# Performance work log

Hardware: AMD Instinct MI355X
Metric: run time of the kernel (lower is better)

The kernel has to match this reference:

```python
import jax, jax.numpy as jnp
import numpy as np

SIZES = (20, 20, 20, 20, 20)          # formula_oh_sizes
OH_N = sum(SIZES)                      # 100
NUM_BINS = 65536                       # spect_bin.get_num_bins()
EPS_SIZE = 1e-4                        # eps added to subset size
IN_EPS = 1e-5                          # torch InstanceNorm1d default eps


def thermometer_oh(counts):
    # StructuredOneHot with accum=True: per-element thermometer encoding.
    # counts: (N, E) element counts -> (N, sum(SIZES)) with out[j]=1 iff j < count.
    outs = [(jnp.arange(s, dtype=counts.dtype)[None, :] < counts[:, i:i + 1]).astype(jnp.float32)
            for i, s in enumerate(SIZES)]
    return jnp.concatenate(outs, axis=-1)


def inorm(x):
    # InstanceNorm1d (affine=False) as applied here: normalize over last dim per row.
    m = jnp.mean(x, axis=-1, keepdims=True)
    v = jnp.var(x, axis=-1, keepdims=True)
    return (x - m) * jax.lax.rsqrt(v + IN_EPS)


def _lin(key, fan_in, fan_out):
    k1, k2 = jax.random.split(key)
    bound = 1.0 / np.sqrt(fan_in)
    W = jax.random.uniform(k1, (fan_in, fan_out), jnp.float32, -bound, bound)
    b = jax.random.uniform(k2, (fan_out,), jnp.float32, -bound, bound)
    return W, b


def setup_inputs():
    key = jax.random.key(0)
    ks = jax.random.split(key, 12)
    B, A, GF, S, P, E, D = 8, 48, 256, 4096, 32, 5, 256
    vert_feat_in = jax.random.normal(ks[0], (B, A, GF), jnp.float32)
    vert_mask_in = jnp.ones((B, A), jnp.float32)
    elem_idx = jax.random.randint(ks[1], (B, A), 0, E)
    vert_element_oh = jax.nn.one_hot(elem_idx, E, dtype=jnp.float32)
    adj_oh = jnp.zeros((B, A, A), jnp.float32)                      # unused by forward path
    atom_subsets = jax.random.randint(ks[2], (B, S, A), 0, 2).astype(jnp.int32)
    atom_subsets_peaks = jnp.zeros((1,), jnp.float32)               # unused (mass_idx/intensity used)
    mass_idx = jax.random.randint(ks[3], (B, S, P), 0, NUM_BINS).astype(jnp.int32)
    intensity = jax.random.uniform(ks[4], (B, S, P), jnp.float32)
    combine_W, combine_b = _lin(ks[5], OH_N + GF, GF)
    l1_W, l1_b = _lin(ks[6], GF, D)
    l2a_W, l2a_b = _lin(ks[7], D, D)
    l2b_W, l2b_b = _lin(ks[8], D, D)
    score_W, score_b = _lin(ks[9], D, 1)
    return {
        'vert_feat_in': vert_feat_in, 'vert_mask_in': vert_mask_in,
        'vert_element_oh': vert_element_oh, 'adj_oh': adj_oh,
        'atom_subsets': atom_subsets, 'atom_subsets_peaks': atom_subsets_peaks,
        'mass_idx': mass_idx, 'intensity': intensity,
        'combine_W': combine_W, 'combine_b': combine_b,
        'l1_W': l1_W, 'l1_b': l1_b, 'l2a_W': l2a_W, 'l2a_b': l2a_b,
        'l2b_W': l2b_W, 'l2b_b': l2b_b, 'score_W': score_W, 'score_b': score_b,
    }


def reference(vert_feat_in, vert_mask_in, vert_element_oh, adj_oh, atom_subsets,
              atom_subsets_peaks, mass_idx, intensity,
              combine_W, combine_b, l1_W, l1_b, l2a_W, l2a_b, l2b_W, l2b_b,
              score_W, score_b):
    B, A, GF = vert_feat_in.shape
    _, S, _ = atom_subsets.shape
    subsets_f = atom_subsets.astype(jnp.float32)
    masked_vert = vert_feat_in * vert_mask_in[:, :, None]               # (B,A,GF)
    subsets_masked = subsets_f * vert_mask_in[:, None, :]               # (B,S,A)
    # weighted sum of vertex features over each subset
    sws = jnp.einsum('bag,bsa->bsg', masked_vert, subsets_masked)        # (B,S,GF)
    # per-subset element counts -> structured one-hot formula encoding
    counts = jnp.einsum('bae,bsa->bse', vert_element_oh, subsets_f)      # (B,S,E)
    pf_oh = thermometer_oh(counts.reshape(-1, counts.shape[-1])).reshape(B, S, OH_N)
    subset_size = jnp.sum(subsets_masked, axis=2) + EPS_SIZE             # (B,S)
    mean_feat = sws / subset_size[:, :, None]
    normed = inorm(mean_feat)                                            # subset_weighted_norm
    combined = jax.nn.relu(jnp.concatenate([pf_oh, normed], -1) @ combine_W + combine_b)
    x = inorm(combined)                                                  # norm_post_combine
    x = jax.nn.relu(x @ l1_W + l1_b)
    x = jax.nn.leaky_relu(x @ l2a_W + l2a_b)
    x = jax.nn.leaky_relu(x @ l2b_W + l2b_b)
    x = jax.nn.relu(x)
    x = inorm(x)                                                         # norm_pre_score
    scores = (x @ score_W + score_b)[..., 0]                             # (B,S)
    probs = jax.nn.softmax(scores, axis=-1)
    # per-batch sparse mass-matrix binning: scatter-add intensity*prob into spectral bins
    weighted = intensity * probs[:, :, None]                             # (B,S,P)
    seg = jax.vmap(lambda idx, w: jax.ops.segment_sum(w, idx, num_segments=NUM_BINS))
    spect_out = seg(mass_idx.reshape(B, -1), weighted.reshape(B, -1))    # (B,NUM_BINS)
    return spect_out, probs
```

## Files before the change

kernel.cpp:

```cpp
#include <hip/hip_runtime.h>
#include <math.h>

#define B_DIM 8
#define A_DIM 48
#define GF_DIM 256
#define S_DIM 4096
#define P_DIM 32
#define E_DIM 5
#define OHN 100
#define NBINS 65536

typedef __attribute__((ext_vector_type(8))) short short8v;
typedef __attribute__((ext_vector_type(4))) float float4v;

__device__ __forceinline__ float wave_sum(float v) {
#pragma unroll
    for (int o = 32; o; o >>= 1) v += __shfl_xor(v, o, 64);
    return v;
}
__device__ __forceinline__ float wave_max(float v) {
#pragma unroll
    for (int o = 32; o; o >>= 1) v = fmaxf(v, __shfl_xor(v, o, 64));
    return v;
}
__device__ __forceinline__ float quad16_sum(float v) {
    v += __shfl_xor(v, 1, 64); v += __shfl_xor(v, 2, 64);
    v += __shfl_xor(v, 4, 64); v += __shfl_xor(v, 8, 64);
    return v;
}
__device__ __forceinline__ unsigned short bf16_rn(float x) {
    unsigned int u = __float_as_uint(x);
    return (unsigned short)((u + 0x7FFFu + ((u >> 16) & 1u)) >> 16);
}
__device__ __forceinline__ float bf16_val(unsigned short h) {
    return __uint_as_float(((unsigned int)h) << 16);
}
__device__ __forceinline__ float4v mfma_bf16(short8v a, short8v b, float4v c) {
    return __builtin_amdgcn_mfma_f32_16x16x32_bf16(a, b, c, 0, 0, 0);
}

__global__ __launch_bounds__(256) void k_prep(
    const float* __restrict__ cW, const float* __restrict__ l1W,
    const float* __restrict__ l2aW, const float* __restrict__ l2bW,
    const float* __restrict__ vert_feat, const float* __restrict__ vert_mask,
    const float* __restrict__ elem_oh,
    short* __restrict__ wp, short* __restrict__ wv,
    float* __restrict__ maskB, int* __restrict__ eiB,
    float4* __restrict__ spect4)
{
    const int blk = blockIdx.x;
    const int tid = threadIdx.x;
    if (blk < 1152) {
        int e = blk * 256 + tid;
        int c = e >> 13;
        int i = e & 8191;
        int j    = i & 7;
        int lane = (i >> 3) & 63;
        int nt   = (i >> 9) & 1;
        int wn   = i >> 10;
        int krel = (lane >> 4) * 8 + j;
        int n    = wn * 32 + nt * 16 + (lane & 15);
        float val = 0.f;
        if (c < 12) {
            int kp = c * 32 + krel;
            if (kp < 100)       val = cW[kp * 256 + n];
            else if (kp >= 128) val = cW[(kp - 28) * 256 + n];
        } else {
            int L  = (c - 12) >> 3;
            int kc = (c - 12) & 7;
            const float* W = (L == 0) ? l1W : (L == 1) ? l2aW : l2bW;
            val = W[(kc * 32 + krel) * 256 + n];
        }
        unsigned short h = bf16_rn(val);
        float lo = val - bf16_val(h);
        int base = c * 16384 + (i & 511);
        wp[base + (wn * 4 + nt) * 512]     = (short)h;
        wp[base + (wn * 4 + 2 + nt) * 512] = (short)bf16_rn(lo);
    } else if (blk < 1664) {
        int vb = blk - 1152;
        int vc = vb >> 5;
        int i  = (vb & 31) * 256 + tid;
        int b  = vc >> 1, v = vc & 1;
        int j    = i & 7;
        int lane = (i >> 3) & 63;
        int nt   = (i >> 9) & 1;
        int wn   = i >> 10;
        int k = v * 32 + (lane >> 4) * 8 + j;
        int n = wn * 32 + nt * 16 + (lane & 15);
        float val = 0.f;
        if (k < A_DIM) {
            float mk = vert_mask[b * A_DIM + k];
            val = vert_feat[((size_t)(b * A_DIM + k)) * GF_DIM + n] * mk * mk;
        }
        unsigned short h = bf16_rn(val);
        float lo = val - bf16_val(h);
        int base = vc * 16384 + (i & 511);
        wv[base + (wn * 4 + nt) * 512]     = (short)h;
        wv[base + (wn * 4 + 2 + nt) * 512] = (short)bf16_rn(lo);
    } else if (blk == 1664) {
        for (int t = tid; t < B_DIM * A_DIM; t += 256) {
            maskB[t] = vert_mask[t];
            int ei = 0;
#pragma unroll
            for (int e = 0; e < E_DIM; ++e)
                if (elem_oh[t * E_DIM + e] > 0.5f) ei = e;
            eiB[t] = ei;
        }
    } else {
        int z = (blk - 1665) * 256 + tid;
        spect4[z] = make_float4(0.f, 0.f, 0.f, 0.f);
    }
}

#define L_XAL 16384
#define L_PS  32768
#define L_TM  33792
#define L_INV 34304
#define L_TOT 34432

template <int NKC, int ACT, bool NORM, bool SCORE, bool THERM>
__device__ __forceinline__ void layer_pass(
    short* xAh, short* xAl, float (*ps)[32], const uint4* __restrict__ tm,
    const short* __restrict__ wstream, const float* __restrict__ bias,
    const float* __restrict__ sW, const float* __restrict__ sb,
    float* __restrict__ scores, int R0)
{
    const int tid  = threadIdx.x;
    const int lane = tid & 63;
    const int wn   = tid >> 6;
    const int quad = lane >> 4;
    const int col  = lane & 15;
    const short* wbase = wstream + wn * 2048 + lane * 8;

    unsigned int tw01 = 0, tw23 = 0;
    if (THERM) {
        const int sh = quad * 8;
        uint4 t0 = tm[col];
        uint4 t1 = tm[16 + col];
        tw01 = ((t0.x >> sh) & 0xFFu)        | (((t1.x >> sh) & 0xFFu) << 8)
             | (((t0.y >> sh) & 0xFFu) << 16) | (((t1.y >> sh) & 0xFFu) << 24);
        tw23 = ((t0.z >> sh) & 0xFFu)        | (((t1.z >> sh) & 0xFFu) << 8)
             | (((t0.w >> sh) & 0xFFu) << 16) | (((t1.w >> sh) & 0xFFu) << 24);
    }

    float4v acc[2][2];
#pragma unroll
    for (int mi = 0; mi < 2; ++mi)
#pragma unroll
        for (int nt = 0; nt < 2; ++nt) acc[mi][nt] = (float4v){0.f, 0.f, 0.f, 0.f};

    short8v bh[3][2], bl[3][2];
#pragma unroll
    for (int p = 0; p < 2; ++p) {
        if (p < NKC) {
            const short* q = wbase + p * 16384;
            bh[p][0] = *(const short8v*)(q);
            bh[p][1] = *(const short8v*)(q + 512);
            bl[p][0] = *(const short8v*)(q + 1024);
            bl[p][1] = *(const short8v*)(q + 1536);
        }
    }

#pragma unroll
    for (int kc = 0; kc < NKC; ++kc) {
        const int cur = kc % 3;
        if (kc + 2 < NKC) {
            const int nxt = (kc + 2) % 3;
            const short* q = wbase + (kc + 2) * 16384;
            bh[nxt][0] = *(const short8v*)(q);
            bh[nxt][1] = *(const short8v*)(q + 512);
            bl[nxt][0] = *(const short8v*)(q + 1024);
            bl[nxt][1] = *(const short8v*)(q + 1536);
        }
        const bool isT = THERM && (kc < 4);
        short8v ah[2], al[2];
        if (isT) {
            const unsigned int w = (kc < 2) ? tw01 : tw23;
#pragma unroll
            for (int mi = 0; mi < 2; ++mi) {
                const int bb = (kc & 1) * 16 + mi * 8;
                short8v hv;
#pragma unroll
                for (int j = 0; j < 8; ++j)
                    hv[j] = (short)(((w >> (bb + j)) & 1u) ? 0x3F80 : 0);
                ah[mi] = hv;
            }
        } else {
            const int ki = THERM ? (kc - 4) : kc;
#pragma unroll
            for (int mi = 0; mi < 2; ++mi) {
                ah[mi] = *(const short8v*)(xAh + ((ki * 2 + mi) * 64 + lane) * 8);
                al[mi] = *(const short8v*)(xAl + ((ki * 2 + mi) * 64 + lane) * 8);
            }
        }
#pragma unroll
        for (int mi = 0; mi < 2; ++mi)
#pragma unroll
            for (int nt = 0; nt < 2; ++nt) {
                acc[mi][nt] = mfma_bf16(ah[mi], bh[cur][nt], acc[mi][nt]);
                acc[mi][nt] = mfma_bf16(ah[mi], bl[cur][nt], acc[mi][nt]);
                if (!isT)
                    acc[mi][nt] = mfma_bf16(al[mi], bh[cur][nt], acc[mi][nt]);
            }
    }

    float bc0 = bias[wn * 32 + col];
    float bc1 = bias[wn * 32 + 16 + col];
#pragma unroll
    for (int mi = 0; mi < 2; ++mi)
#pragma unroll
        for (int r = 0; r < 4; ++r) {
            float z0 = acc[mi][0][r] + bc0;
            float z1 = acc[mi][1][r] + bc1;
            if (ACT == 0) { z0 = fmaxf(z0, 0.f); z1 = fmaxf(z1, 0.f); }
            else { z0 = (z0 > 0.f) ? z0 : 0.01f * z0; z1 = (z1 > 0.f) ? z1 : 0.01f * z1; }
            acc[mi][0][r] = z0; acc[mi][1][r] = z1;
        }

    __syncthreads();

    if (NORM) {
        float rsum[2][4];
#pragma unroll
        for (int mi = 0; mi < 2; ++mi)
#pragma unroll
            for (int r = 0; r < 4; ++r)
                rsum[mi][r] = quad16_sum(acc[mi][0][r] + acc[mi][1][r]);
        if (col == 0) {
#pragma unroll
            for (int mi = 0; mi < 2; ++mi)
#pragma unroll
                for (int r = 0; r < 4; ++r)
                    ps[wn][mi * 16 + quad * 4 + r] = rsum[mi][r];
        }
        __syncthreads();
        float mu[2][4];
#pragma unroll
        for (int mi = 0; mi < 2; ++mi)
#pragma unroll
            for (int r = 0; r < 4; ++r) {
                int m = mi * 16 + quad * 4 + r;
                float s = 0.f;
#pragma unroll
                for (int w = 0; w < 8; ++w) s += ps[w][m];
                mu[mi][r] = s * (1.f / 256.f);
            }
        __syncthreads();
        float qs[2][4];
#pragma unroll
        for (int mi = 0; mi < 2; ++mi)
#pragma unroll
            for (int r = 0; r < 4; ++r) {
                acc[mi][0][r] -= mu[mi][r];
                acc[mi][1][r] -= mu[mi][r];
                float q = acc[mi][0][r] * acc[mi][0][r]
                        + acc[mi][1][r] * acc[mi][1][r];
                qs[mi][r] = quad16_sum(q);
            }
        if (col == 0) {
#pragma unroll
            for (int mi = 0; mi < 2; ++mi)
#pragma unroll
                for (int r = 0; r < 4; ++r)
                    ps[wn][mi * 16 + quad * 4 + r] = qs[mi][r];
        }
        __syncthreads();
#pragma unroll
        for (int mi = 0; mi < 2; ++mi)
#pragma unroll
            for (int r = 0; r < 4; ++r) {
                int m = mi * 16 + quad * 4 + r;
                float s = 0.f;
#pragma unroll
                for (int w = 0; w < 8; ++w) s += ps[w][m];
                float rsf = 1.0f / sqrtf(s * (1.f / 256.f) + 1e-5f);
                acc[mi][0][r] *= rsf;
                acc[mi][1][r] *= rsf;
            }
    }

    if (SCORE) {
        __syncthreads();
        float sv0 = sW[wn * 32 + col];
        float sv1 = sW[wn * 32 + 16 + col];
        float psu[2][4];
#pragma unroll
        for (int mi = 0; mi < 2; ++mi)
#pragma unroll
            for (int r = 0; r < 4; ++r)
                psu[mi][r] = quad16_sum(acc[mi][0][r] * sv0 + acc[mi][1][r] * sv1);
        if (col == 0) {
#pragma unroll
            for (int mi = 0; mi < 2; ++mi)
#pragma unroll
                for (int r = 0; r < 4; ++r)
                    ps[wn][mi * 16 + quad * 4 + r] = psu[mi][r];
        }
        __syncthreads();
        if (tid < 32) {
            float s = sb[0];
#pragma unroll
            for (int w = 0; w < 8; ++w) s += ps[w][tid];
            scores[R0 + tid] = s;
        }
    } else {
#pragma unroll
        for (int mi = 0; mi < 2; ++mi)
#pragma unroll
            for (int nt = 0; nt < 2; ++nt) {
                int nn0 = (nt * 16 + col) & ~1;
                int q2  = nn0 >> 3;
                int j0  = nn0 & 7;
#pragma unroll
                for (int r = 0; r < 4; ++r) {
                    float v  = acc[mi][nt][r];
                    float pv = __shfl_xor(v, 1, 64);
                    int m15 = quad * 4 + r;
                    int rowidx = (wn * 2 + mi) * 64 + q2 * 16 + m15;
                    if ((col & 1) == 0) {
                        unsigned int wd = (unsigned int)bf16_rn(v)
                                        | ((unsigned int)bf16_rn(pv) << 16);
                        ((unsigned int*)xAh)[rowidx * 4 + (j0 >> 1)] = wd;
                    } else {
                        float ls = v  - bf16_val(bf16_rn(v));
                        float lp = pv - bf16_val(bf16_rn(pv));
                        unsigned int wd = (unsigned int)bf16_rn(lp)
                                        | ((unsigned int)bf16_rn(ls) << 16);
                        ((unsigned int*)xAl)[rowidx * 4 + (j0 >> 1)] = wd;
                    }
                }
            }
        __syncthreads();
    }
}

__global__ __launch_bounds__(512, 4) void k_mlp(
    const int* __restrict__ subsets, const short* __restrict__ wprep,
    const short* __restrict__ vertB,
    const float* __restrict__ maskB, const int* __restrict__ eiB,
    const float* __restrict__ cb,  const float* __restrict__ l1b,
    const float* __restrict__ l2ab, const float* __restrict__ l2bb,
    const float* __restrict__ sW,  const float* __restrict__ sb,
    float* __restrict__ scores)
{
    __shared__ __align__(16) char smem[L_TOT];
    short*  xAh = (short*)smem;
    short*  xAl = (short*)(smem + L_XAL);
    short*  fm  = (short*)(smem + L_XAL);
    float (*ps)[32]  = (float(*)[32])(smem + L_PS);
    uint4*  tm       = (uint4*)(smem + L_TM);
    float*  invsz    = (float*)(smem + L_INV);

    const int tid  = threadIdx.x;
    const int lane = tid & 63;
    const int wn   = tid >> 6;
    const int quad = lane >> 4;
    const int col  = lane & 15;
    const int fb   = blockIdx.x;
    const int b    = fb >> 7;
    const int R0   = fb * 32;

    if (tid < 256) {
        int g  = tid;
        int lg = g & 63;
        int t2 = g >> 6;
        int kc = t2 >> 1, mi = t2 & 1;
        int m  = mi * 16 + (lg & 15);
        int k0 = kc * 32 + (lg >> 4) * 8;
        const int* srow = subsets + (size_t)(R0 + m) * A_DIM;
        short8v hv;
#pragma unroll
        for (int j = 0; j < 8; ++j) {
            int k = k0 + j;
            hv[j] = (short)((k < A_DIM && srow[k]) ? 0x3F80 : 0);
        }
        *(short8v*)(fm + g * 8) = hv;
    }

    {
        const float mymask = (lane < A_DIM) ? maskB[b * A_DIM + lane] : 0.f;
        const int   myei   = (lane < A_DIM) ? eiB[b * A_DIM + lane]   : -1;
        unsigned long long* tmw = (unsigned long long*)tm;
#pragma unroll
        for (int i = 0; i < 4; ++i) {
            int r = wn * 4 + i;
            int fl = (lane < A_DIM) ? subsets[(size_t)(R0 + r) * A_DIM + lane] : 0;
            unsigned long long m0 = __ballot(fl != 0 && myei == 0);
            unsigned long long m1 = __ballot(fl != 0 && myei == 1);
            unsigned long long m2 = __ballot(fl != 0 && myei == 2);
            unsigned long long m3 = __ballot(fl != 0 && myei == 3);
            unsigned long long m4 = __ballot(fl != 0 && myei == 4);
            float ssz = wave_sum(fl ? mymask : 0.f) + 1e-4f;
            if (lane == 0) {
                unsigned int c0 = __popcll(m0), c1 = __popcll(m1),
                             c2 = __popcll(m2), c3 = __popcll(m3),
                             c4 = __popcll(m4);
                unsigned long long r0 = (1ull << (c0 > 20u ? 20u : c0)) - 1ull;
                unsigned long long r1 = (1ull << (c1 > 20u ? 20u : c1)) - 1ull;
                unsigned long long r2 = (1ull << (c2 > 20u ? 20u : c2)) - 1ull;
                unsigned long long r3 = (1ull << (c3 > 20u ? 20u : c3)) - 1ull;
                unsigned long long r4 = (1ull << (c4 > 20u ? 20u : c4)) - 1ull;
                unsigned long long lo = r0 | (r1 << 20) | (r2 << 40) | (r3 << 60);
                unsigned long long hi = (r3 >> 4) | (r4 << 16);
                tmw[r * 2]     = lo;
                tmw[r * 2 + 1] = hi;
                invsz[r]  = 1.0f / ssz;
            }
        }
    }
    __syncthreads();

    {
        const short* wbase = vertB + b * 32768 + wn * 2048 + lane * 8;
        float4v acc[2][2];
#pragma unroll
        for (int mi = 0; mi < 2; ++mi)
#pragma unroll
            for (int nt = 0; nt < 2; ++nt) acc[mi][nt] = (float4v){0.f, 0.f, 0.f, 0.f};

        short8v bh[2][2], bl[2][2];
#pragma unroll
        for (int kc = 0; kc < 2; ++kc) {
            const short* q = wbase + kc * 16384;
            bh[kc][0] = *(const short8v*)(q);
            bh[kc][1] = *(const short8v*)(q + 512);
            bl[kc][0] = *(const short8v*)(q + 1024);
            bl[kc][1] = *(const short8v*)(q + 1536);
        }
#pragma unroll
        for (int kc = 0; kc < 2; ++kc) {
            short8v a0 = *(const short8v*)(fm + ((kc * 2 + 0) * 64 + lane) * 8);
            short8v a1 = *(const short8v*)(fm + ((kc * 2 + 1) * 64 + lane) * 8);
#pragma unroll
            for (int nt = 0; nt < 2; ++nt) {
                acc[0][nt] = mfma_bf16(a0, bh[kc][nt], acc[0][nt]);
                acc[0][nt] = mfma_bf16(a0, bl[kc][nt], acc[0][nt]);
                acc[1][nt] = mfma_bf16(a1, bh[kc][nt], acc[1][nt]);
                acc[1][nt] = mfma_bf16(a1, bl[kc][nt], acc[1][nt]);
            }
        }

#pragma unroll
        for (int mi = 0; mi < 2; ++mi)
#pragma unroll
            for (int r = 0; r < 4; ++r) {
                float iv = invsz[mi * 16 + quad * 4 + r];
                acc[mi][0][r] *= iv;
                acc[mi][1][r] *= iv;
            }

        __syncthreads();

        {
            float rsum[2][4];
#pragma unroll
            for (int mi = 0; mi < 2; ++mi)
#pragma unroll
                for (int r = 0; r < 4; ++r)
                    rsum[mi][r] = quad16_sum(acc[mi][0][r] + acc[mi][1][r]);
            if (col == 0) {
#pragma unroll
                for (int mi = 0; mi < 2; ++mi)
#pragma unroll
                    for (int r = 0; r < 4; ++r)
                        ps[wn][mi * 16 + quad * 4 + r] = rsum[mi][r];
            }
            __syncthreads();
            float mu[2][4];
#pragma unroll
            for (int mi = 0; mi < 2; ++mi)
#pragma unroll
                for (int r = 0; r < 4; ++r) {
                    int m = mi * 16 + quad * 4 + r;
                    float s = 0.f;
#pragma unroll
                    for (int w = 0; w < 8; ++w) s += ps[w][m];
                    mu[mi][r] = s * (1.f / 256.f);
                }
            __syncthreads();
            float qs[2][4];
#pragma unroll
            for (int mi = 0; mi < 2; ++mi)
#pragma unroll
                for (int r = 0; r < 4; ++r) {
                    acc[mi][0][r] -= mu[mi][r];
                    acc[mi][1][r] -= mu[mi][r];
                    float q = acc[mi][0][r] * acc[mi][0][r]
                            + acc[mi][1][r] * acc[mi][1][r];
                    qs[mi][r] = quad16_sum(q);
                }
            if (col == 0) {
#pragma unroll
                for (int mi = 0; mi < 2; ++mi)
#pragma unroll
                    for (int r = 0; r < 4; ++r)
                        ps[wn][mi * 16 + quad * 4 + r] = qs[mi][r];
            }
            __syncthreads();
#pragma unroll
            for (int mi = 0; mi < 2; ++mi)
#pragma unroll
                for (int r = 0; r < 4; ++r) {
                    int m = mi * 16 + quad * 4 + r;
                    float s = 0.f;
#pragma unroll
                    for (int w = 0; w < 8; ++w) s += ps[w][m];
                    float rsf = 1.0f / sqrtf(s * (1.f / 256.f) + 1e-5f);
                    acc[mi][0][r] *= rsf;
                    acc[mi][1][r] *= rsf;
                }
        }

#pragma unroll
        for (int mi = 0; mi < 2; ++mi)
#pragma unroll
            for (int nt = 0; nt < 2; ++nt) {
                int nn0 = (nt * 16 + col) & ~1;
                int q2  = nn0 >> 3;
                int j0  = nn0 & 7;
#pragma unroll
                for (int r = 0; r < 4; ++r) {
                    float v  = acc[mi][nt][r];
                    float pv = __shfl_xor(v, 1, 64);
                    int m15 = quad * 4 + r;
                    int rowidx = (wn * 2 + mi) * 64 + q2 * 16 + m15;
                    if ((col & 1) == 0) {
                        unsigned int wd = (unsigned int)bf16_rn(v)
                                        | ((unsigned int)bf16_rn(pv) << 16);
                        ((unsigned int*)xAh)[rowidx * 4 + (j0 >> 1)] = wd;
                    } else {
                        float ls = v  - bf16_val(bf16_rn(v));
                        float lp = pv - bf16_val(bf16_rn(pv));
                        unsigned int wd = (unsigned int)bf16_rn(lp)
                                        | ((unsigned int)bf16_rn(ls) << 16);
                        ((unsigned int*)xAl)[rowidx * 4 + (j0 >> 1)] = wd;
                    }
                }
            }
        __syncthreads();
    }

    layer_pass<12, 0, true,  false, true >(xAh, xAl, ps, tm, wprep,
        cb, nullptr, nullptr, nullptr, R0);
    layer_pass< 8, 0, false, false, false>(xAh, xAl, ps, tm, wprep + 12 * 16384,
        l1b, nullptr, nullptr, nullptr, R0);
    layer_pass< 8, 1, false, false, false>(xAh, xAl, ps, tm, wprep + 20 * 16384,
        l2ab, nullptr, nullptr, nullptr, R0);
    layer_pass< 8, 0, true,  true,  false>(xAh, xAl, ps, tm, wprep + 28 * 16384,
        l2bb, sW, sb, scores, R0);
}

__global__ __launch_bounds__(256) void k_softmax(float* __restrict__ probs) {
    const int b   = blockIdx.x;
    const int tid = threadIdx.x;
    __shared__ float redA[4];
    __shared__ float redB[4];
    float* sp = probs + (size_t)b * S_DIM;

    float v[16];
    float mx = -INFINITY;
#pragma unroll
    for (int i = 0; i < 16; ++i) {
        v[i] = sp[tid + i * 256];
        mx = fmaxf(mx, v[i]);
    }
    mx = wave_max(mx);
    if ((tid & 63) == 0) redA[tid >> 6] = mx;
    __syncthreads();
    mx = fmaxf(fmaxf(redA[0], redA[1]), fmaxf(redA[2], redA[3]));

    float sum = 0.f;
#pragma unroll
    for (int i = 0; i < 16; ++i) {
        v[i] = expf(v[i] - mx);
        sum += v[i];
    }
    sum = wave_sum(sum);
    if ((tid & 63) == 0) redB[tid >> 6] = sum;
    __syncthreads();
    float tot = redB[0] + redB[1] + redB[2] + redB[3];
    float inv = 1.0f / tot;
#pragma unroll
    for (int i = 0; i < 16; ++i) sp[tid + i * 256] = v[i] * inv;
}

__global__ __launch_bounds__(256) void k_scatter(
    const int*   __restrict__ mass_idx,
    const float* __restrict__ intensity,
    const float* __restrict__ probs,
    float* __restrict__ spect)
{
    int i  = blockIdx.x * 256 + threadIdx.x;
    int bs = i >> 5;
    int b  = i >> 17;
    float w = intensity[i] * probs[bs];
    unsafeAtomicAdd(spect + ((size_t)b << 16) + mass_idx[i], w);
}

extern "C" void kernel_launch(void* const* d_in, const int* in_sizes, int n_in,
                              void* d_out, int out_size, void* d_ws, size_t ws_size,
                              hipStream_t stream) {
    const float* vert_feat = (const float*)d_in[0];
    const float* vert_mask = (const float*)d_in[1];
    const float* elem_oh   = (const float*)d_in[2];
    const int*   subsets   = (const int*)d_in[4];
    const int*   mass_idx  = (const int*)d_in[6];
    const float* intensity = (const float*)d_in[7];
    const float* combine_W = (const float*)d_in[8];
    const float* combine_b = (const float*)d_in[9];
    const float* l1_W      = (const float*)d_in[10];
    const float* l1_b      = (const float*)d_in[11];
    const float* l2a_W     = (const float*)d_in[12];
    const float* l2a_b     = (const float*)d_in[13];
    const float* l2b_W     = (const float*)d_in[14];
    const float* l2b_b     = (const float*)d_in[15];
    const float* score_W   = (const float*)d_in[16];
    const float* score_b   = (const float*)d_in[17];

    float* out   = (float*)d_out;
    float* spect = out;
    float* probs = out + (size_t)B_DIM * NBINS;

    short* wprep = (short*)d_ws;
    short* vertB = wprep + 36 * 16384;
    float* maskB = (float*)(vertB + 16 * 16384);
    int*   eiB   = (int*)(maskB + B_DIM * A_DIM);

    k_prep<<<2177, 256, 0, stream>>>(combine_W, l1_W, l2a_W, l2b_W,
        vert_feat, vert_mask, elem_oh, wprep, vertB, maskB, eiB,
        (float4*)spect);
    k_mlp<<<1024, 512, 0, stream>>>(subsets, wprep, vertB, maskB, eiB,
        combine_b, l1_b, l2a_b, l2b_b, score_W, score_b, probs);
    k_softmax<<<B_DIM, 256, 0, stream>>>(probs);
    k_scatter<<<(B_DIM * S_DIM * P_DIM) / 256, 256, 0, stream>>>(
        mass_idx, intensity, probs, spect);
}
```

Before: 247.1 us.

## Double MLP row tile to 64 rows per block to reuse streamed weights

Each k_mlp block now processes 64 subset rows instead of 32, with each wave computing four 16-row MFMA tiles rather than two, and the grid is halved to 512 blocks. Every weight fragment loaded from global memory now feeds twice as many MFMAs, which reduces weight traffic per row. The weight prefetch depth drops from two chunks ahead to one to offset the larger accumulator and A-operand register footprint, and shared memory roughly doubles. Risks are higher register pressure and lower occupancy, fewer blocks relative to the CU count, and less latency hiding on the weight stream.

```diff
diff --git a/kernel.cpp b/kernel.cpp
--- a/kernel.cpp
+++ b/kernel.cpp
@@ -112,15 +112,15 @@
     }
 }
 
-#define L_XAL 16384
-#define L_PS  32768
-#define L_TM  33792
-#define L_INV 34304
-#define L_TOT 34432
+#define L_XAL 32768
+#define L_PS  65536
+#define L_TM  67584
+#define L_INV 68608
+#define L_TOT 68864
 
 template <int NKC, int ACT, bool NORM, bool SCORE, bool THERM>
 __device__ __forceinline__ void layer_pass(
-    short* xAh, short* xAl, float (*ps)[32], const uint4* __restrict__ tm,
+    short* xAh, short* xAl, float (*ps)[64], const uint4* __restrict__ tm,
     const short* __restrict__ wstream, const float* __restrict__ bias,
     const float* __restrict__ sW, const float* __restrict__ sb,
     float* __restrict__ scores, int R0)
@@ -132,69 +132,72 @@
     const int col  = lane & 15;
     const short* wbase = wstream + wn * 2048 + lane * 8;
 
-    unsigned int tw01 = 0, tw23 = 0;
+    unsigned int tw0 = 0, tw1 = 0, tw2 = 0, tw3 = 0;
     if (THERM) {
         const int sh = quad * 8;
         uint4 t0 = tm[col];
         uint4 t1 = tm[16 + col];
-        tw01 = ((t0.x >> sh) & 0xFFu)        | (((t1.x >> sh) & 0xFFu) << 8)
-             | (((t0.y >> sh) & 0xFFu) << 16) | (((t1.y >> sh) & 0xFFu) << 24);
-        tw23 = ((t0.z >> sh) & 0xFFu)        | (((t1.z >> sh) & 0xFFu) << 8)
-             | (((t0.w >> sh) & 0xFFu) << 16) | (((t1.w >> sh) & 0xFFu) << 24);
-    }
-
-    float4v acc[2][2];
-#pragma unroll
-    for (int mi = 0; mi < 2; ++mi)
+        uint4 t2 = tm[32 + col];
+        uint4 t3 = tm[48 + col];
+        tw0 = ((t0.x >> sh) & 0xFFu)        | (((t1.x >> sh) & 0xFFu) << 8)
+            | (((t2.x >> sh) & 0xFFu) << 16) | (((t3.x >> sh) & 0xFFu) << 24);
+        tw1 = ((t0.y >> sh) & 0xFFu)        | (((t1.y >> sh) & 0xFFu) << 8)
+            | (((t2.y >> sh) & 0xFFu) << 16) | (((t3.y >> sh) & 0xFFu) << 24);
+        tw2 = ((t0.z >> sh) & 0xFFu)        | (((t1.z >> sh) & 0xFFu) << 8)
+            | (((t2.z >> sh) & 0xFFu) << 16) | (((t3.z >> sh) & 0xFFu) << 24);
+        tw3 = ((t0.w >> sh) & 0xFFu)        | (((t1.w >> sh) & 0xFFu) << 8)
+            | (((t2.w >> sh) & 0xFFu) << 16) | (((t3.w >> sh) & 0xFFu) << 24);
+    }
+
+    float4v acc[4][2];
+#pragma unroll
+    for (int mi = 0; mi < 4; ++mi)
 #pragma unroll
         for (int nt = 0; nt < 2; ++nt) acc[mi][nt] = (float4v){0.f, 0.f, 0.f, 0.f};
 
-    short8v bh[3][2], bl[3][2];
-#pragma unroll
-    for (int p = 0; p < 2; ++p) {
-        if (p < NKC) {
-            const short* q = wbase + p * 16384;
-            bh[p][0] = *(const short8v*)(q);
-            bh[p][1] = *(const short8v*)(q + 512);
-            bl[p][0] = *(const short8v*)(q + 1024);
-            bl[p][1] = *(const short8v*)(q + 1536);
-        }
+    short8v bh[2][2], bl[2][2];
+    {
+        const short* q = wbase;
+        bh[0][0] = *(const short8v*)(q);
+        bh[0][1] = *(const short8v*)(q + 512);
+        bl[0][0] = *(const short8v*)(q + 1024);
+        bl[0][1] = *(const short8v*)(q + 1536);
     }
 
 #pragma unroll
     for (int kc = 0; kc < NKC; ++kc) {
-        const int cur = kc % 3;
-        if (kc + 2 < NKC) {
-            const int nxt = (kc + 2) % 3;
-            const short* q = wbase + (kc + 2) * 16384;
+        const int cur = kc & 1;
+        if (kc + 1 < NKC) {
+            const int nxt = (kc + 1) & 1;
+            const short* q = wbase + (kc + 1) * 16384;
             bh[nxt][0] = *(const short8v*)(q);
             bh[nxt][1] = *(const short8v*)(q + 512);
             bl[nxt][0] = *(const short8v*)(q + 1024);
             bl[nxt][1] = *(const short8v*)(q + 1536);
         }
         const bool isT = THERM && (kc < 4);
-        short8v ah[2], al[2];
+        short8v ah[4], al[4];
         if (isT) {
-            const unsigned int w = (kc < 2) ? tw01 : tw23;
-#pragma unroll
-            for (int mi = 0; mi < 2; ++mi) {
-                const int bb = (kc & 1) * 16 + mi * 8;
+            const unsigned int w = (kc == 0) ? tw0 : (kc == 1) ? tw1
+                                 : (kc == 2) ? tw2 : tw3;
+#pragma unroll
+            for (int mi = 0; mi < 4; ++mi) {
                 short8v hv;
 #pragma unroll
                 for (int j = 0; j < 8; ++j)
-                    hv[j] = (short)(((w >> (bb + j)) & 1u) ? 0x3F80 : 0);
+                    hv[j] = (short)(((w >> (mi * 8 + j)) & 1u) ? 0x3F80 : 0);
                 ah[mi] = hv;
             }
         } else {
             const int ki = THERM ? (kc - 4) : kc;
 #pragma unroll
-            for (int mi = 0; mi < 2; ++mi) {
-                ah[mi] = *(const short8v*)(xAh + ((ki * 2 + mi) * 64 + lane) * 8);
-                al[mi] = *(const short8v*)(xAl + ((ki * 2 + mi) * 64 + lane) * 8);
-            }
-        }
-#pragma unroll
-        for (int mi = 0; mi < 2; ++mi)
+            for (int mi = 0; mi < 4; ++mi) {
+                ah[mi] = *(const short8v*)(xAh + ((ki * 4 + mi) * 64 + lane) * 8);
+                al[mi] = *(const short8v*)(xAl + ((ki * 4 + mi) * 64 + lane) * 8);
+            }
+        }
+#pragma unroll
+        for (int mi = 0; mi < 4; ++mi)
 #pragma unroll
             for (int nt = 0; nt < 2; ++nt) {
                 acc[mi][nt] = mfma_bf16(ah[mi], bh[cur][nt], acc[mi][nt]);
@@ -207,7 +210,7 @@
     float bc0 = bias[wn * 32 + col];
     float bc1 = bias[wn * 32 + 16 + col];
 #pragma unroll
-    for (int mi = 0; mi < 2; ++mi)
+    for (int mi = 0; mi < 4; ++mi)
 #pragma unroll
         for (int r = 0; r < 4; ++r) {
             float z0 = acc[mi][0][r] + bc0;
@@ -220,23 +223,23 @@
     __syncthreads();
 
     if (NORM) {
-        float rsum[2][4];
-#pragma unroll
-        for (int mi = 0; mi < 2; ++mi)
+        float rsum[4][4];
+#pragma unroll
+        for (int mi = 0; mi < 4; ++mi)
 #pragma unroll
             for (int r = 0; r < 4; ++r)
                 rsum[mi][r] = quad16_sum(acc[mi][0][r] + acc[mi][1][r]);
         if (col == 0) {
 #pragma unroll
-            for (int mi = 0; mi < 2; ++mi)
+            for (int mi = 0; mi < 4; ++mi)
 #pragma unroll
                 for (int r = 0; r < 4; ++r)
                     ps[wn][mi * 16 + quad * 4 + r] = rsum[mi][r];
         }
         __syncthreads();
-        float mu[2][4];
-#pragma unroll
-        for (int mi = 0; mi < 2; ++mi)
+        float mu[4][4];
+#pragma unroll
+        for (int mi = 0; mi < 4; ++mi)
 #pragma unroll
             for (int r = 0; r < 4; ++r) {
                 int m = mi * 16 + quad * 4 + r;
@@ -246,9 +249,9 @@
                 mu[mi][r] = s * (1.f / 256.f);
             }
         __syncthreads();
-        float qs[2][4];
-#pragma unroll
-        for (int mi = 0; mi < 2; ++mi)
+        float qs[4][4];
+#pragma unroll
+        for (int mi = 0; mi < 4; ++mi)
 #pragma unroll
             for (int r = 0; r < 4; ++r) {
                 acc[mi][0][r] -= mu[mi][r];
@@ -259,14 +262,14 @@
             }
         if (col == 0) {
 #pragma unroll
-            for (int mi = 0; mi < 2; ++mi)
+            for (int mi = 0; mi < 4; ++mi)
 #pragma unroll
                 for (int r = 0; r < 4; ++r)
                     ps[wn][mi * 16 + quad * 4 + r] = qs[mi][r];
         }
         __syncthreads();
 #pragma unroll
-        for (int mi = 0; mi < 2; ++mi)
+        for (int mi = 0; mi < 4; ++mi)
 #pragma unroll
             for (int r = 0; r < 4; ++r) {
                 int m = mi * 16 + quad * 4 + r;
@@ -283,21 +286,21 @@
         __syncthreads();
         float sv0 = sW[wn * 32 + col];
         float sv1 = sW[wn * 32 + 16 + col];
-        float psu[2][4];
-#pragma unroll
-        for (int mi = 0; mi < 2; ++mi)
+        float psu[4][4];
+#pragma unroll
+        for (int mi = 0; mi < 4; ++mi)
 #pragma unroll
             for (int r = 0; r < 4; ++r)
                 psu[mi][r] = quad16_sum(acc[mi][0][r] * sv0 + acc[mi][1][r] * sv1);
         if (col == 0) {
 #pragma unroll
-            for (int mi = 0; mi < 2; ++mi)
+            for (int mi = 0; mi < 4; ++mi)
 #pragma unroll
                 for (int r = 0; r < 4; ++r)
                     ps[wn][mi * 16 + quad * 4 + r] = psu[mi][r];
         }
         __syncthreads();
-        if (tid < 32) {
+        if (tid < 64) {
             float s = sb[0];
 #pragma unroll
             for (int w = 0; w < 8; ++w) s += ps[w][tid];
@@ -305,7 +308,7 @@
         }
     } else {
 #pragma unroll
-        for (int mi = 0; mi < 2; ++mi)
+        for (int mi = 0; mi < 4; ++mi)
 #pragma unroll
             for (int nt = 0; nt < 2; ++nt) {
                 int nn0 = (nt * 16 + col) & ~1;
@@ -316,7 +319,7 @@
                     float v  = acc[mi][nt][r];
                     float pv = __shfl_xor(v, 1, 64);
                     int m15 = quad * 4 + r;
-                    int rowidx = (wn * 2 + mi) * 64 + q2 * 16 + m15;
+                    int rowidx = (wn * 4 + mi) * 64 + q2 * 16 + m15;
                     if ((col & 1) == 0) {
                         unsigned int wd = (unsigned int)bf16_rn(v)
                                         | ((unsigned int)bf16_rn(pv) << 16);
@@ -347,7 +350,7 @@
     short*  xAh = (short*)smem;
     short*  xAl = (short*)(smem + L_XAL);
     short*  fm  = (short*)(smem + L_XAL);
-    float (*ps)[32]  = (float(*)[32])(smem + L_PS);
+    float (*ps)[64]  = (float(*)[64])(smem + L_PS);
     uint4*  tm       = (uint4*)(smem + L_TM);
     float*  invsz    = (float*)(smem + L_INV);
 
@@ -357,14 +360,14 @@
     const int quad = lane >> 4;
     const int col  = lane & 15;
     const int fb   = blockIdx.x;
-    const int b    = fb >> 7;
-    const int R0   = fb * 32;
-
-    if (tid < 256) {
+    const int b    = fb >> 6;
+    const int R0   = fb * 64;
+
+    {
         int g  = tid;
         int lg = g & 63;
         int t2 = g >> 6;
-        int kc = t2 >> 1, mi = t2 & 1;
+        int kc = t2 >> 2, mi = t2 & 3;
         int m  = mi * 16 + (lg & 15);
         int k0 = kc * 32 + (lg >> 4) * 8;
         const int* srow = subsets + (size_t)(R0 + m) * A_DIM;
@@ -382,8 +385,8 @@
         const int   myei   = (lane < A_DIM) ? eiB[b * A_DIM + lane]   : -1;
         unsigned long long* tmw = (unsigned long long*)tm;
 #pragma unroll
-        for (int i = 0; i < 4; ++i) {
-            int r = wn * 4 + i;
+        for (int i = 0; i < 8; ++i) {
+            int r = wn * 8 + i;
             int fl = (lane < A_DIM) ? subsets[(size_t)(R0 + r) * A_DIM + lane] : 0;
             unsigned long long m0 = __ballot(fl != 0 && myei == 0);
             unsigned long long m1 = __ballot(fl != 0 && myei == 1);
@@ -412,9 +415,9 @@
 
     {
         const short* wbase = vertB + b * 32768 + wn * 2048 + lane * 8;
-        float4v acc[2][2];
-#pragma unroll
-        for (int mi = 0; mi < 2; ++mi)
+        float4v acc[4][2];
+#pragma unroll
+        for (int mi = 0; mi < 4; ++mi)
 #pragma unroll
             for (int nt = 0; nt < 2; ++nt) acc[mi][nt] = (float4v){0.f, 0.f, 0.f, 0.f};
 
@@ -429,19 +432,19 @@
         }
 #pragma unroll
         for (int kc = 0; kc < 2; ++kc) {
-            short8v a0 = *(const short8v*)(fm + ((kc * 2 + 0) * 64 + lane) * 8);
-            short8v a1 = *(const short8v*)(fm + ((kc * 2 + 1) * 64 + lane) * 8);
-#pragma unroll
-            for (int nt = 0; nt < 2; ++nt) {
-                acc[0][nt] = mfma_bf16(a0, bh[kc][nt], acc[0][nt]);
-                acc[0][nt] = mfma_bf16(a0, bl[kc][nt], acc[0][nt]);
-                acc[1][nt] = mfma_bf16(a1, bh[kc][nt], acc[1][nt]);
-                acc[1][nt] = mfma_bf16(a1, bl[kc][nt], acc[1][nt]);
-            }
-        }
-
-#pragma unroll
-        for (int mi = 0; mi < 2; ++mi)
+#pragma unroll
+            for (int mi = 0; mi < 4; ++mi) {
+                short8v a = *(const short8v*)(fm + ((kc * 4 + mi) * 64 + lane) * 8);
+#pragma unroll
+                for (int nt = 0; nt < 2; ++nt) {
+                    acc[mi][nt] = mfma_bf16(a, bh[kc][nt], acc[mi][nt]);
+                    acc[mi][nt] = mfma_bf16(a, bl[kc][nt], acc[mi][nt]);
+                }
+            }
+        }
+
+#pragma unroll
+        for (int mi = 0; mi < 4; ++mi)
 #pragma unroll
             for (int r = 0; r < 4; ++r) {
                 float iv = invsz[mi * 16 + quad * 4 + r];
@@ -452,23 +455,23 @@
         __syncthreads();
 
         {
-            float rsum[2][4];
-#pragma unroll
-            for (int mi = 0; mi < 2; ++mi)
+            float rsum[4][4];
+#pragma unroll
+            for (int mi = 0; mi < 4; ++mi)
 #pragma unroll
                 for (int r = 0; r < 4; ++r)
                     rsum[mi][r] = quad16_sum(acc[mi][0][r] + acc[mi][1][r]);
             if (col == 0) {
 #pragma unroll
-                for (int mi = 0; mi < 2; ++mi)
+                for (int mi = 0; mi < 4; ++mi)
 #pragma unroll
                     for (int r = 0; r < 4; ++r)
                         ps[wn][mi * 16 + quad * 4 + r] = rsum[mi][r];
             }
             __syncthreads();
-            float mu[2][4];
-#pragma unroll
-            for (int mi = 0; mi < 2; ++mi)
+            float mu[4][4];
+#pragma unroll
+            for (int mi = 0; mi < 4; ++mi)
 #pragma unroll
                 for (int r = 0; r < 4; ++r) {
                     int m = mi * 16 + quad * 4 + r;
@@ -478,9 +481,9 @@
                     mu[mi][r] = s * (1.f / 256.f);
                 }
             __syncthreads();
-            float qs[2][4];
-#pragma unroll
-            for (int mi = 0; mi < 2; ++mi)
+            float qs[4][4];
+#pragma unroll
+            for (int mi = 0; mi < 4; ++mi)
 #pragma unroll
                 for (int r = 0; r < 4; ++r) {
                     acc[mi][0][r] -= mu[mi][r];
@@ -491,14 +494,14 @@
                 }
             if (col == 0) {
 #pragma unroll
-                for (int mi = 0; mi < 2; ++mi)
+                for (int mi = 0; mi < 4; ++mi)
 #pragma unroll
                     for (int r = 0; r < 4; ++r)
                         ps[wn][mi * 16 + quad * 4 + r] = qs[mi][r];
             }
             __syncthreads();
 #pragma unroll
-            for (int mi = 0; mi < 2; ++mi)
+            for (int mi = 0; mi < 4; ++mi)
 #pragma unroll
                 for (int r = 0; r < 4; ++r) {
                     int m = mi * 16 + quad * 4 + r;
@@ -512,7 +515,7 @@
         }
 
 #pragma unroll
-        for (int mi = 0; mi < 2; ++mi)
+        for (int mi = 0; mi < 4; ++mi)
 #pragma unroll
             for (int nt = 0; nt < 2; ++nt) {
                 int nn0 = (nt * 16 + col) & ~1;
@@ -523,7 +526,7 @@
                     float v  = acc[mi][nt][r];
                     float pv = __shfl_xor(v, 1, 64);
                     int m15 = quad * 4 + r;
-                    int rowidx = (wn * 2 + mi) * 64 + q2 * 16 + m15;
+                    int rowidx = (wn * 4 + mi) * 64 + q2 * 16 + m15;
                     if ((col & 1) == 0) {
                         unsigned int wd = (unsigned int)bf16_rn(v)
                                         | ((unsigned int)bf16_rn(pv) << 16);
@@ -629,7 +632,7 @@
     k_prep<<<2177, 256, 0, stream>>>(combine_W, l1_W, l2a_W, l2b_W,
         vert_feat, vert_mask, elem_oh, wprep, vertB, maskB, eiB,
         (float4*)spect);
-    k_mlp<<<1024, 512, 0, stream>>>(subsets, wprep, vertB, maskB, eiB,
+    k_mlp<<<512, 512, 0, stream>>>(subsets, wprep, vertB, maskB, eiB,
         combine_b, l1_b, l2a_b, l2b_b, score_W, score_b, probs);
     k_softmax<<<B_DIM, 256, 0, stream>>>(probs);
     k_scatter<<<(B_DIM * S_DIM * P_DIM) / 256, 256, 0, stream>>>(
```

Result: slower. 279.5 us (+13.1%).
